# Optimization experiments

Hardware: AMD Instinct MI355X
Metric: run time of the kernel (lower is better)

## Reference

```python
import jax, jax.numpy as jnp
import numpy as np

B, N, HID = 8, 512, 512
HEADS, HD = 16, 32
FFN, DEMB = 2048, 64
EPS = 1e-5


def layer_norm(x, g, b):
    mu = jnp.mean(x, axis=-1, keepdims=True)
    var = jnp.var(x, axis=-1, keepdims=True)
    return (x - mu) * jax.lax.rsqrt(var + EPS) * g + b


def setup_inputs() -> dict:
    key = jax.random.key(0)
    ks = jax.random.split(key, 16)
    s = lambda fan_in: 1.0 / np.sqrt(fan_in)
    return {
        "x": jax.random.normal(ks[0], (B, N, HID), jnp.float32),
        "distance_features": jax.random.normal(ks[1], (B, N, N, DEMB), jnp.float32),
        "edge_mask": jax.random.randint(ks[2], (B, N, N), 0, 2) > 0,
        "qkv_w": jax.random.uniform(ks[3], (HID, 3 * HID), jnp.float32, -s(HID), s(HID)),
        "qkv_b": jnp.zeros((3 * HID,), jnp.float32),
        "out_w": jax.random.uniform(ks[4], (HID, HID), jnp.float32, -s(HID), s(HID)),
        "out_b": jnp.zeros((HID,), jnp.float32),
        "dist_w": jax.random.uniform(ks[5], (DEMB, HEADS), jnp.float32, -s(DEMB), s(DEMB)),
        "dist_b": jnp.zeros((HEADS,), jnp.float32),
        "ln1_g": jnp.ones((HID,), jnp.float32),
        "ln1_b": jnp.zeros((HID,), jnp.float32),
        "ln2_g": jnp.ones((HID,), jnp.float32),
        "ln2_b": jnp.zeros((HID,), jnp.float32),
        "ff1_w": jax.random.uniform(ks[6], (HID, FFN), jnp.float32, -s(HID), s(HID)),
        "ff1_b": jnp.zeros((FFN,), jnp.float32),
        "ff2_w": jax.random.uniform(ks[7], (FFN, HID), jnp.float32, -s(FFN), s(FFN)),
        "ff2_b": jnp.zeros((HID,), jnp.float32),
    }


def reference(x, distance_features, edge_mask, qkv_w, qkv_b, out_w, out_b,
              dist_w, dist_b, ln1_g, ln1_b, ln2_g, ln2_b,
              ff1_w, ff1_b, ff2_w, ff2_b):
    residual = x
    h = layer_norm(x, ln1_g, ln1_b)
    qkv = h @ qkv_w + qkv_b  # [B,N,3*HID]
    q, k, v = jnp.split(qkv, 3, axis=-1)
    q = q.reshape(B, N, HEADS, HD)
    k = k.reshape(B, N, HEADS, HD)
    v = v.reshape(B, N, HEADS, HD)
    scale = jnp.sqrt(jnp.float32(HD))
    scores = jnp.einsum('bihd,bjhd->bhij', q, k) / scale  # [B,H,N,N]
    bias = distance_features @ dist_w + dist_b  # [B,N,N,H]
    scores = scores + jnp.transpose(bias, (0, 3, 1, 2))
    neg = jnp.finfo(scores.dtype).min
    scores = jnp.where(edge_mask[:, None, :, :], scores, neg)
    attn = jax.nn.softmax(scores, axis=-1)
    ctx = jnp.einsum('bhij,bjhd->bihd', attn, v).reshape(B, N, HID)
    x = residual + ctx @ out_w + out_b
    y = layer_norm(x, ln2_g, ln2_b)
    ff = jax.nn.gelu(y @ ff1_w + ff1_b, approximate=False) @ ff2_w + ff2_b
    return x + ff
```

## Files before the change

### kernel.cpp

```cpp
#include <hip/hip_runtime.h>
#include <cstddef>
#include <cstdint>

#define B_     8
#define N_     512
#define HID_   512
#define HEADS_ 16
#define HD_    32
#define FFN_   2048
#define DEMB_  64
#define ROWS   (B_*N_)

typedef unsigned short u16;
typedef short bf16x8 __attribute__((ext_vector_type(8)));
typedef float f32x4  __attribute__((ext_vector_type(4)));
typedef short short8v __attribute__((ext_vector_type(8)));
typedef short short4v __attribute__((ext_vector_type(4)));

__device__ __forceinline__ u16 f2bf(float f) {
  unsigned u = __float_as_uint(f);
  u += 0x7fffu + ((u >> 16) & 1u);
  return (u16)(u >> 16);
}
__device__ __forceinline__ float bf2f(u16 b) {
  return __uint_as_float(((unsigned)b) << 16);
}

__device__ __forceinline__ void gload16(const void* g, void* l) {
  __builtin_amdgcn_global_load_lds(
      (const __attribute__((address_space(1))) unsigned int*)g,
      (__attribute__((address_space(3))) unsigned int*)l, 16, 0, 0);
}

__device__ __forceinline__ void wt_tile(const float* __restrict__ W,
                                        u16* __restrict__ Wt,
                                        int K, int N, int tt, int tid) {
  __shared__ float tile[32][33];
  const int nt = N / 32;
  const int n0 = (tt % nt) * 32, k0 = (tt / nt) * 32;
  const int tx = tid & 31, ty = tid >> 5;
  #pragma unroll
  for (int i = 0; i < 4; ++i)
    tile[ty + 8 * i][tx] = W[(size_t)(k0 + ty + 8 * i) * N + n0 + tx];
  __syncthreads();
  #pragma unroll
  for (int i = 0; i < 4; ++i) {
    const int n = ty + 8 * i;
    Wt[(size_t)(n0 + n) * K + k0 + tx] = f2bf(tile[tx][n]);
  }
}

__global__ __launch_bounds__(256) void prep_kernel(
    const float* __restrict__ qkv_w, const float* __restrict__ out_w,
    const float* __restrict__ ff1_w, const float* __restrict__ ff2_w,
    u16* __restrict__ qkv_wt, u16* __restrict__ out_wt,
    u16* __restrict__ ff1_wt, u16* __restrict__ ff2_wt,
    const unsigned char* __restrict__ mask, int* __restrict__ flag) {
  const int bid = blockIdx.x, t = threadIdx.x;
  if (bid < 768) {
    wt_tile(qkv_w, qkv_wt, HID_, 3 * HID_, bid, t);
  } else if (bid < 1024) {
    wt_tile(out_w, out_wt, HID_, HID_, bid - 768, t);
  } else if (bid < 2048) {
    wt_tile(ff1_w, ff1_wt, HID_, FFN_, bid - 1024, t);
  } else if (bid < 3072) {
    wt_tile(ff2_w, ff2_wt, FFN_, HID_, bid - 2048, t);
  } else {
    const int idx = (bid - 3072) * 256 + t;
    if ((idx & 3) != 0 && mask[idx] != 0) atomicOr(flag, 1);
  }
}

__global__ __launch_bounds__(256) void ln_kernel(const float* __restrict__ x,
                                                 const float* __restrict__ g,
                                                 const float* __restrict__ bt,
                                                 u16* __restrict__ y) {
  const int lane = threadIdx.x & 63;
  const int row  = blockIdx.x * 4 + (threadIdx.x >> 6);
  const float* xr = x + (size_t)row * HID_;
  float4 v0 = *(const float4*)(xr + lane * 8);
  float4 v1 = *(const float4*)(xr + lane * 8 + 4);
  float s = v0.x + v0.y + v0.z + v0.w + v1.x + v1.y + v1.z + v1.w;
  float q = v0.x*v0.x + v0.y*v0.y + v0.z*v0.z + v0.w*v0.w
          + v1.x*v1.x + v1.y*v1.y + v1.z*v1.z + v1.w*v1.w;
  #pragma unroll
  for (int off = 32; off > 0; off >>= 1) {
    s += __shfl_xor(s, off, 64);
    q += __shfl_xor(q, off, 64);
  }
  const float mean = s * (1.0f / HID_);
  const float var  = q * (1.0f / HID_) - mean * mean;
  const float rs   = rsqrtf(var + 1e-5f);
  const float4 g0 = *(const float4*)(g + lane * 8);
  const float4 g1 = *(const float4*)(g + lane * 8 + 4);
  const float4 b0 = *(const float4*)(bt + lane * 8);
  const float4 b1 = *(const float4*)(bt + lane * 8 + 4);
  short8v o;
  o[0] = (short)f2bf((v0.x - mean) * rs * g0.x + b0.x);
  o[1] = (short)f2bf((v0.y - mean) * rs * g0.y + b0.y);
  o[2] = (short)f2bf((v0.z - mean) * rs * g0.z + b0.z);
  o[3] = (short)f2bf((v0.w - mean) * rs * g0.w + b0.w);
  o[4] = (short)f2bf((v1.x - mean) * rs * g1.x + b1.x);
  o[5] = (short)f2bf((v1.y - mean) * rs * g1.y + b1.y);
  o[6] = (short)f2bf((v1.z - mean) * rs * g1.z + b1.z);
  o[7] = (short)f2bf((v1.w - mean) * rs * g1.w + b1.w);
  *(short8v*)(y + (size_t)row * HID_ + lane * 8) = o;
}

template <int ACT, bool HAS_RES, bool OUT_BF16>
__global__ __launch_bounds__(256) void mfma_gemm(
    const u16* __restrict__ A, const u16* __restrict__ Wt,
    const float* __restrict__ bias, const float* __restrict__ res,
    void* __restrict__ Cout, int N, int K) {
  __shared__ __align__(16) u16 As[128 * 64];
  __shared__ __align__(16) u16 Bs[128 * 64];
  const int t    = threadIdx.x;
  const int wid  = t >> 6, lane = t & 63;
  const int wr   = wid >> 1, wc = wid & 1;
  const int m0   = blockIdx.y * 128, n0 = blockIdx.x * 128;
  const int srow8 = lane >> 3;
  const int sslot = (lane & 7) ^ srow8;

  f32x4 zero = {0.f, 0.f, 0.f, 0.f};
  f32x4 acc[4][4];
  #pragma unroll
  for (int m = 0; m < 4; ++m)
    #pragma unroll
    for (int n = 0; n < 4; ++n) acc[m][n] = zero;

  for (int kt = 0; kt < K; kt += 64) {
    __syncthreads();
    #pragma unroll
    for (int i = 0; i < 4; ++i) {
      const int rbase = wid * 32 + i * 8;
      const int r = rbase + srow8;
      gload16(A  + (size_t)(m0 + r) * K + kt + sslot * 8, &As[rbase * 64]);
      gload16(Wt + (size_t)(n0 + r) * K + kt + sslot * 8, &Bs[rbase * 64]);
    }
    __syncthreads();
    #pragma unroll
    for (int kk = 0; kk < 2; ++kk) {
      bf16x8 a[4], b[4];
      #pragma unroll
      for (int m = 0; m < 4; ++m) {
        const int row = wr * 64 + m * 16 + (lane & 15);
        const int s   = (kk * 4 + (lane >> 4)) ^ (row & 7);
        a[m] = *(const bf16x8*)&As[row * 64 + s * 8];
      }
      #pragma unroll
      for (int n = 0; n < 4; ++n) {
        const int row = wc * 64 + n * 16 + (lane & 15);
        const int s   = (kk * 4 + (lane >> 4)) ^ (row & 7);
        b[n] = *(const bf16x8*)&Bs[row * 64 + s * 8];
      }
      #pragma unroll
      for (int m = 0; m < 4; ++m)
        #pragma unroll
        for (int n = 0; n < 4; ++n)
          acc[m][n] = __builtin_amdgcn_mfma_f32_16x16x32_bf16(
              a[m], b[n], acc[m][n], 0, 0, 0);
    }
  }
  #pragma unroll
  for (int n = 0; n < 4; ++n) {
    const int col = n0 + wc * 64 + n * 16 + (lane & 15);
    const float bb = bias[col];
    #pragma unroll
    for (int m = 0; m < 4; ++m) {
      #pragma unroll
      for (int j = 0; j < 4; ++j) {
        const int row = m0 + wr * 64 + m * 16 + (lane >> 4) * 4 + j;
        float v = acc[m][n][j] + bb;
        if (ACT == 1) v = 0.5f * v * (1.0f + erff(v * 0.70710678118654752f));
        const size_t off = (size_t)row * N + col;
        if (HAS_RES) v += res[off];
        if (OUT_BF16) ((u16*)Cout)[off] = f2bf(v);
        else          ((float*)Cout)[off] = v;
      }
    }
  }
}

__global__ __launch_bounds__(256) void bias_kernel(
    const float* __restrict__ df, const unsigned char* __restrict__ mask8,
    const float* __restrict__ dw, const float* __restrict__ db,
    const int* __restrict__ flag, u16* __restrict__ biasb) {
  __shared__ float dfs[128][68];
  __shared__ u16 obuf[HEADS_][128];
  __shared__ unsigned char mbuf[128];
  const int t    = threadIdx.x;
  const int tile = blockIdx.x & 3;
  const int i    = (blockIdx.x >> 2) & 511;
  const int b    = blockIdx.x >> 11;
  const int j0   = tile * 128;
  const int h    = t >> 4;
  const int jt   = t & 15;

  const float4* gsrc =
      (const float4*)(df + (((size_t)b * N_ + i) * N_ + j0) * DEMB_);
  #pragma unroll
  for (int s = 0; s < 8; ++s) {
    const int f   = s * 256 + t;
    *(float4*)&dfs[f >> 4][(f & 15) * 4] = gsrc[f];
  }
  const int fb = *flag;
  if (t < 128) {
    const size_t midx = ((size_t)b * N_ + i) * N_ + j0 + t;
    mbuf[t] = fb ? (mask8[midx] != 0) : (((const int*)mask8)[midx] != 0);
  }

  float4 w[16];
  #pragma unroll
  for (int d4 = 0; d4 < 16; ++d4) {
    w[d4].x = dw[(d4 * 4 + 0) * HEADS_ + h];
    w[d4].y = dw[(d4 * 4 + 1) * HEADS_ + h];
    w[d4].z = dw[(d4 * 4 + 2) * HEADS_ + h];
    w[d4].w = dw[(d4 * 4 + 3) * HEADS_ + h];
  }
  const float bh = db[h];
  __syncthreads();

  #pragma unroll
  for (int s = 0; s < 8; ++s) {
    const int jl = s * 16 + jt;
    float a0 = 0.f, a1 = 0.f, a2 = 0.f, a3 = 0.f;
    #pragma unroll
    for (int d4 = 0; d4 < 16; ++d4) {
      const float4 v = *(const float4*)&dfs[jl][d4 * 4];
      a0 += v.x * w[d4].x;
      a1 += v.y * w[d4].y;
      a2 += v.z * w[d4].z;
      a3 += v.w * w[d4].w;
    }
    const float acc = (a0 + a1) + (a2 + a3) + bh;
    obuf[h][jl] = f2bf(mbuf[jl] ? acc : -1e30f);
  }
  __syncthreads();
  const int h2 = t >> 4, c = t & 15;
  u16* ob = biasb + (((size_t)b * HEADS_ + h2) * N_ + i) * N_ + j0;
  *(short8v*)(ob + c * 8) = *(const short8v*)&obuf[h2][c * 8];
}

__global__ __launch_bounds__(256) void attn_kernel(
    const float* __restrict__ qkv, const u16* __restrict__ biasb,
    u16* __restrict__ ctx) {
  __shared__ union {
    u16 k[N_ * HD_];
    struct {
      float po[3][64][33];
      float pm[3][64];
      float pl[3][64];
    } c;
  } sm;
  const int t    = threadIdx.x;
  const int bx   = blockIdx.x;
  const int b    = bx >> 7;
  const int h    = (bx >> 3) & 15;
  const int iblk = bx & 7;
  const int jq   = t >> 6;
  const int r    = t & 63;
  const int i    = iblk * 64 + r;
  const size_t qbase = (size_t)b * N_ * (3 * HID_);

  for (int idx = t; idx < N_ * 8; idx += 256) {
    const int j = idx >> 3, f = idx & 7;
    const float4 kv = *(const float4*)(qkv + qbase + (size_t)j * (3 * HID_) +
                                       HID_ + h * HD_ + f * 4);
    short4v ks;
    ks[0] = (short)f2bf(kv.x); ks[1] = (short)f2bf(kv.y);
    ks[2] = (short)f2bf(kv.z); ks[3] = (short)f2bf(kv.w);
    *(short4v*)&sm.k[j * HD_ + f * 4] = ks;
  }
  __syncthreads();

  float q[HD_];
  {
    const float* qp = qkv + qbase + (size_t)i * (3 * HID_) + h * HD_;
    #pragma unroll
    for (int f = 0; f < 8; ++f) {
      const float4 v = *(const float4*)(qp + f * 4);
      q[f*4+0] = v.x * 0.17677669529663687f;
      q[f*4+1] = v.y * 0.17677669529663687f;
      q[f*4+2] = v.z * 0.17677669529663687f;
      q[f*4+3] = v.w * 0.17677669529663687f;
    }
  }
  const u16* brow = biasb + (((size_t)b * HEADS_ + h) * N_ + i) * N_ + jq * 128;
  const float* vbase = qkv + qbase + 2 * HID_ + h * HD_;
  float m = -3.0e38f, l = 0.f;
  float o[HD_];
  #pragma unroll
  for (int d = 0; d < HD_; ++d) o[d] = 0.f;

  for (int j8 = 0; j8 < 128; j8 += 8) {
    const short8v bq = *(const short8v*)(brow + j8);
    #pragma unroll
    for (int e = 0; e < 8; ++e) {
      const int j = jq * 128 + j8 + e;
      const u16* kr = &sm.k[j * HD_];
      float s = 0.f;
      #pragma unroll
      for (int c = 0; c < 4; ++c) {
        const short8v kk = *(const short8v*)(kr + c * 8);
        #pragma unroll
        for (int d = 0; d < 8; ++d)
          s += q[c*8+d] * bf2f((u16)kk[d]);
      }
      s += bf2f((u16)bq[e]);
      if (s - m > 8.0f) {
        const float corr = __expf(m - s);
        l *= corr;
        #pragma unroll
        for (int d = 0; d < HD_; ++d) o[d] *= corr;
        m = s;
      }
      const float p = __expf(s - m);
      l += p;
      const float4* vr = (const float4*)(vbase + (size_t)j * (3 * HID_));
      #pragma unroll
      for (int c = 0; c < 8; ++c) {
        const float4 vv = vr[c];
        o[c*4+0] += p * vv.x; o[c*4+1] += p * vv.y;
        o[c*4+2] += p * vv.z; o[c*4+3] += p * vv.w;
      }
    }
  }

  __syncthreads();
  if (jq > 0) {
    sm.c.pm[jq-1][r] = m;
    sm.c.pl[jq-1][r] = l;
    #pragma unroll
    for (int d = 0; d < HD_; ++d) sm.c.po[jq-1][r][d] = o[d];
  }
  __syncthreads();
  if (jq == 0) {
    #pragma unroll
    for (int p2 = 0; p2 < 3; ++p2) {
      const float m2 = sm.c.pm[p2][r], l2 = sm.c.pl[p2][r];
      const float mn = fmaxf(m, m2);
      const float c1 = __expf(m - mn), c2 = __expf(m2 - mn);
      l = l * c1 + l2 * c2;
      #pragma unroll
      for (int d = 0; d < HD_; ++d)
        o[d] = o[d] * c1 + sm.c.po[p2][r][d] * c2;
      m = mn;
    }
    const float inv = 1.0f / l;
    u16* cp = ctx + (((size_t)b * N_ + i) * HEADS_ + h) * HD_;
    #pragma unroll
    for (int f = 0; f < 4; ++f) {
      short8v v;
      #pragma unroll
      for (int e = 0; e < 8; ++e) v[e] = (short)f2bf(o[f*8+e] * inv);
      *(short8v*)(cp + f * 8) = v;
    }
  }
}

extern "C" void kernel_launch(void* const* d_in, const int* in_sizes, int n_in,
                              void* d_out, int out_size, void* d_ws, size_t ws_size,
                              hipStream_t stream) {
  const float* x      = (const float*)d_in[0];
  const float* df     = (const float*)d_in[1];
  const unsigned char* mask = (const unsigned char*)d_in[2];
  const float* qkv_w  = (const float*)d_in[3];
  const float* qkv_b  = (const float*)d_in[4];
  const float* out_w  = (const float*)d_in[5];
  const float* out_b  = (const float*)d_in[6];
  const float* dist_w = (const float*)d_in[7];
  const float* dist_b = (const float*)d_in[8];
  const float* ln1_g  = (const float*)d_in[9];
  const float* ln1_b  = (const float*)d_in[10];
  const float* ln2_g  = (const float*)d_in[11];
  const float* ln2_b  = (const float*)d_in[12];
  const float* ff1_w  = (const float*)d_in[13];
  const float* ff1_b  = (const float*)d_in[14];
  const float* ff2_w  = (const float*)d_in[15];
  const float* ff2_b  = (const float*)d_in[16];
  float* out = (float*)d_out;

  char* p = (char*)d_ws;
  auto alloc = [&](size_t bytes) {
    char* r = p;
    p += (bytes + 255) & ~(size_t)255;
    return r;
  };
  float* qkv    = (float*)alloc((size_t)ROWS * 3 * HID_ * 4);
  u16*   biasb  = (u16*)alloc((size_t)B_ * HEADS_ * N_ * N_ * 2);
  float* xa     = (float*)alloc((size_t)ROWS * HID_ * 4);
  u16*   h16    = (u16*)alloc((size_t)ROWS * HID_ * 2);
  u16*   ctx16  = (u16*)alloc((size_t)ROWS * HID_ * 2);
  u16*   y16    = (u16*)alloc((size_t)ROWS * HID_ * 2);
  u16*   ff116  = (u16*)alloc((size_t)ROWS * FFN_ * 2);
  u16*   qkv_wt = (u16*)alloc((size_t)3 * HID_ * HID_ * 2);
  u16*   out_wt = (u16*)alloc((size_t)HID_ * HID_ * 2);
  u16*   ff1_wt = (u16*)alloc((size_t)FFN_ * HID_ * 2);
  u16*   ff2_wt = (u16*)alloc((size_t)HID_ * FFN_ * 2);
  int*   flag   = (int*)alloc(sizeof(int));

  hipMemsetAsync(flag, 0, sizeof(int), stream);
  prep_kernel<<<3328, 256, 0, stream>>>(qkv_w, out_w, ff1_w, ff2_w,
                                        qkv_wt, out_wt, ff1_wt, ff2_wt,
                                        mask, flag);
  ln_kernel<<<ROWS / 4, 256, 0, stream>>>(x, ln1_g, ln1_b, h16);
  mfma_gemm<0, false, false><<<dim3(3 * HID_ / 128, ROWS / 128), 256, 0, stream>>>(
      h16, qkv_wt, qkv_b, nullptr, qkv, 3 * HID_, HID_);
  bias_kernel<<<B_ * N_ * 4, 256, 0, stream>>>(df, mask, dist_w, dist_b, flag, biasb);
  attn_kernel<<<B_ * HEADS_ * 8, 256, 0, stream>>>(qkv, biasb, ctx16);
  mfma_gemm<0, true, false><<<dim3(HID_ / 128, ROWS / 128), 256, 0, stream>>>(
      ctx16, out_wt, out_b, x, xa, HID_, HID_);
  ln_kernel<<<ROWS / 4, 256, 0, stream>>>(xa, ln2_g, ln2_b, y16);
  mfma_gemm<1, false, true><<<dim3(FFN_ / 128, ROWS / 128), 256, 0, stream>>>(
      y16, ff1_wt, ff1_b, nullptr, ff116, FFN_, HID_);
  mfma_gemm<0, true, false><<<dim3(HID_ / 128, ROWS / 128), 256, 0, stream>>>(
      ff116, ff2_wt, ff2_b, xa, out, HID_, FFN_);
}
```

Before: 465.2 us.

## Double-buffer GEMM LDS tiles and compute distance bias with MFMA

The GEMM kernel now ping-pongs two LDS buffers, issuing the next K-tile's global-to-LDS loads before the MFMAs on the current tile, with one barrier per step instead of two. The distance-bias kernel stages the distance features with direct global-to-LDS loads into an XOR-swizzled layout. It also replaces the scalar FP32 dot products with bf16 MFMA against the projection weights held in LDS. This targets the bandwidth-bound 512 MB feature read and the per-thread ALU work, at the cost of double the GEMM LDS footprint and bf16 rounding of the bias inputs.

```diff
diff --git a/kernel.cpp b/kernel.cpp
--- a/kernel.cpp
+++ b/kernel.cpp
@@ -112,8 +112,8 @@
     const u16* __restrict__ A, const u16* __restrict__ Wt,
     const float* __restrict__ bias, const float* __restrict__ res,
     void* __restrict__ Cout, int N, int K) {
-  __shared__ __align__(16) u16 As[128 * 64];
-  __shared__ __align__(16) u16 Bs[128 * 64];
+  __shared__ __align__(16) u16 As[2][128 * 64];
+  __shared__ __align__(16) u16 Bs[2][128 * 64];
   const int t    = threadIdx.x;
   const int wid  = t >> 6, lane = t & 63;
   const int wr   = wid >> 1, wc = wid & 1;
@@ -128,16 +128,22 @@
     #pragma unroll
     for (int n = 0; n < 4; ++n) acc[m][n] = zero;
 
-  for (int kt = 0; kt < K; kt += 64) {
-    __syncthreads();
+  auto stage = [&](int buf, int kt) {
     #pragma unroll
     for (int i = 0; i < 4; ++i) {
       const int rbase = wid * 32 + i * 8;
       const int r = rbase + srow8;
-      gload16(A  + (size_t)(m0 + r) * K + kt + sslot * 8, &As[rbase * 64]);
-      gload16(Wt + (size_t)(n0 + r) * K + kt + sslot * 8, &Bs[rbase * 64]);
-    }
-    __syncthreads();
+      gload16(A  + (size_t)(m0 + r) * K + kt + sslot * 8, &As[buf][rbase * 64]);
+      gload16(Wt + (size_t)(n0 + r) * K + kt + sslot * 8, &Bs[buf][rbase * 64]);
+    }
+  };
+
+  const int nsteps = K >> 6;
+  stage(0, 0);
+  __syncthreads();
+  int cur = 0;
+  for (int step = 0; step < nsteps; ++step) {
+    if (step + 1 < nsteps) stage(cur ^ 1, (step + 1) * 64);
     #pragma unroll
     for (int kk = 0; kk < 2; ++kk) {
       bf16x8 a[4], b[4];
@@ -145,13 +151,13 @@
       for (int m = 0; m < 4; ++m) {
         const int row = wr * 64 + m * 16 + (lane & 15);
         const int s   = (kk * 4 + (lane >> 4)) ^ (row & 7);
-        a[m] = *(const bf16x8*)&As[row * 64 + s * 8];
+        a[m] = *(const bf16x8*)&As[cur][row * 64 + s * 8];
       }
       #pragma unroll
       for (int n = 0; n < 4; ++n) {
         const int row = wc * 64 + n * 16 + (lane & 15);
         const int s   = (kk * 4 + (lane >> 4)) ^ (row & 7);
-        b[n] = *(const bf16x8*)&Bs[row * 64 + s * 8];
+        b[n] = *(const bf16x8*)&Bs[cur][row * 64 + s * 8];
       }
       #pragma unroll
       for (int m = 0; m < 4; ++m)
@@ -160,6 +166,8 @@
           acc[m][n] = __builtin_amdgcn_mfma_f32_16x16x32_bf16(
               a[m], b[n], acc[m][n], 0, 0, 0);
     }
+    __syncthreads();
+    cur ^= 1;
   }
   #pragma unroll
   for (int n = 0; n < 4; ++n) {
@@ -185,56 +193,73 @@
     const float* __restrict__ df, const unsigned char* __restrict__ mask8,
     const float* __restrict__ dw, const float* __restrict__ db,
     const int* __restrict__ flag, u16* __restrict__ biasb) {
-  __shared__ float dfs[128][68];
-  __shared__ u16 obuf[HEADS_][128];
+  __shared__ __align__(16) float dfs[128 * 64];
+  __shared__ float wls[64 * 16];
+  __shared__ float dbs[16];
   __shared__ unsigned char mbuf[128];
+  __shared__ u16 obuf[16][132];
+
   const int t    = threadIdx.x;
+  const int wid  = t >> 6, lane = t & 63;
   const int tile = blockIdx.x & 3;
   const int i    = (blockIdx.x >> 2) & 511;
   const int b    = blockIdx.x >> 11;
   const int j0   = tile * 128;
-  const int h    = t >> 4;
-  const int jt   = t & 15;
-
-  const float4* gsrc =
-      (const float4*)(df + (((size_t)b * N_ + i) * N_ + j0) * DEMB_);
+
+  const size_t dfbase = (((size_t)b * N_ + i) * N_ + j0) * DEMB_;
   #pragma unroll
   for (int s = 0; s < 8; ++s) {
-    const int f   = s * 256 + t;
-    *(float4*)&dfs[f >> 4][(f & 15) * 4] = gsrc[f];
-  }
+    const int r0 = wid * 32 + s * 4;
+    const int r  = r0 + (lane >> 4);
+    const int g  = (lane & 15) ^ (r & 15);
+    gload16(df + dfbase + (size_t)r * DEMB_ + g * 4, &dfs[r0 * 64]);
+  }
+  *(float4*)&wls[t * 4] = ((const float4*)dw)[t];
+  if (t < 16) dbs[t] = db[t];
   const int fb = *flag;
   if (t < 128) {
     const size_t midx = ((size_t)b * N_ + i) * N_ + j0 + t;
     mbuf[t] = fb ? (mask8[midx] != 0) : (((const int*)mask8)[midx] != 0);
   }
-
-  float4 w[16];
-  #pragma unroll
-  for (int d4 = 0; d4 < 16; ++d4) {
-    w[d4].x = dw[(d4 * 4 + 0) * HEADS_ + h];
-    w[d4].y = dw[(d4 * 4 + 1) * HEADS_ + h];
-    w[d4].z = dw[(d4 * 4 + 2) * HEADS_ + h];
-    w[d4].w = dw[(d4 * 4 + 3) * HEADS_ + h];
-  }
-  const float bh = db[h];
-  __syncthreads();
-
-  #pragma unroll
-  for (int s = 0; s < 8; ++s) {
-    const int jl = s * 16 + jt;
-    float a0 = 0.f, a1 = 0.f, a2 = 0.f, a3 = 0.f;
-    #pragma unroll
-    for (int d4 = 0; d4 < 16; ++d4) {
-      const float4 v = *(const float4*)&dfs[jl][d4 * 4];
-      a0 += v.x * w[d4].x;
-      a1 += v.y * w[d4].y;
-      a2 += v.z * w[d4].z;
-      a3 += v.w * w[d4].w;
-    }
-    const float acc = (a0 + a1) + (a2 + a3) + bh;
-    obuf[h][jl] = f2bf(mbuf[jl] ? acc : -1e30f);
-  }
+  __syncthreads();
+
+  bf16x8 bw[2];
+  #pragma unroll
+  for (int kk = 0; kk < 2; ++kk)
+    #pragma unroll
+    for (int e = 0; e < 8; ++e) {
+      const int k = kk * 32 + (lane >> 4) * 8 + e;
+      bw[kk][e] = (short)f2bf(wls[k * 16 + (lane & 15)]);
+    }
+
+  f32x4 acc[2] = {{0.f,0.f,0.f,0.f},{0.f,0.f,0.f,0.f}};
+  #pragma unroll
+  for (int t8 = 0; t8 < 2; ++t8) {
+    const int row = wid * 32 + t8 * 16 + (lane & 15);
+    #pragma unroll
+    for (int kk = 0; kk < 2; ++kk) {
+      bf16x8 a;
+      #pragma unroll
+      for (int gg = 0; gg < 2; ++gg) {
+        const int G = kk * 8 + (lane >> 4) * 2 + gg;
+        const int p = G ^ (row & 15);
+        const float4 v = *(const float4*)&dfs[row * 64 + p * 4];
+        a[gg*4+0] = (short)f2bf(v.x); a[gg*4+1] = (short)f2bf(v.y);
+        a[gg*4+2] = (short)f2bf(v.z); a[gg*4+3] = (short)f2bf(v.w);
+      }
+      acc[t8] = __builtin_amdgcn_mfma_f32_16x16x32_bf16(a, bw[kk], acc[t8], 0, 0, 0);
+    }
+  }
+
+  const int h = lane & 15;
+  #pragma unroll
+  for (int t8 = 0; t8 < 2; ++t8)
+    #pragma unroll
+    for (int j = 0; j < 4; ++j) {
+      const int jl = wid * 32 + t8 * 16 + (lane >> 4) * 4 + j;
+      const float v = acc[t8][j] + dbs[h];
+      obuf[h][jl] = f2bf(mbuf[jl] ? v : -1e30f);
+    }
   __syncthreads();
   const int h2 = t >> 4, c = t & 15;
   u16* ob = biasb + (((size_t)b * HEADS_ + h2) * N_ + i) * N_ + j0;
```

Measured after the change: 457.5 us. Within noise of the previous version (-1.7%).
